# Kernel optimization log

Measured on AMD Instinct MI355X. Metric: run time of the kernel, lower is better.

The kernel has to match this reference:

```python
import jax, jax.numpy as jnp
import numpy as np

EMBED = 256
HEADS = 8
HEAD_DIM = EMBED // HEADS
K = 7          # kernel_size
DIL = 1        # dilation
PAD = DIL * (K - 1) // 2  # 3
B, H, W = 4, 56, 56


def setup_inputs() -> dict:
    key = jax.random.key(0)
    ks = jax.random.split(key, 9)
    d = {"x": jax.random.normal(ks[0], (B, H, W, EMBED), jnp.float32)}
    for i, name in enumerate(["wq", "wk", "wv", "wo"]):
        d[name] = jax.random.normal(ks[1 + i], (EMBED, EMBED), jnp.float32) * 0.02
    for i, name in enumerate(["bq", "bk", "bv", "bo"]):
        d[name] = jax.random.normal(ks[5 + i], (EMBED,), jnp.float32) * 0.02
    return d


def _unfold(t):
    # t: [N, d, H, W] -> [N, d, K*K, H, W]; zero padding (matches F.unfold),
    # so out-of-bounds neighbors contribute logit 0, NOT -inf (faithful to source).
    h, w = t.shape[2], t.shape[3]
    tp = jnp.pad(t, ((0, 0), (0, 0), (PAD, PAD), (PAD, PAD)))
    patches = [tp[:, :, i * DIL:i * DIL + h, j * DIL:j * DIL + w]
               for i in range(K) for j in range(K)]  # fixed K*K=49 offsets
    return jnp.stack(patches, axis=2)


def reference(x, wq, bq, wk, bk, wv, bv, wo, bo):
    b, h, w, c = x.shape
    scale = HEAD_DIM ** -0.5
    q = x @ wq.T + bq
    k = x @ wk.T + bk
    v = x @ wv.T + bv

    def to_nh(t):  # [B,H,W,C] -> [B*heads, head_dim, H, W]
        return t.reshape(b, h, w, HEADS, HEAD_DIM).transpose(0, 3, 4, 1, 2).reshape(b * HEADS, HEAD_DIM, h, w)

    q, k, v = to_nh(q), to_nh(k), to_nh(v)
    k_unf = _unfold(k)  # [N, d, K2, H, W]
    v_unf = _unfold(v)
    logits = jnp.einsum('ndhw,ndkhw->nkhw', q, k_unf) * scale  # [N, K2, H, W]
    attn = jax.nn.softmax(logits, axis=1)
    out = jnp.einsum('nkhw,ndkhw->ndhw', attn, v_unf)  # [N, d, H, W]
    out = out.reshape(b, HEADS, HEAD_DIM, h, w).transpose(0, 3, 4, 1, 2).reshape(b, h, w, c)
    return out @ wo.T + bo
```

## Files before the change

### kernel.cpp

```cpp
#include <hip/hip_runtime.h>

typedef unsigned int u32;
typedef unsigned short u16;
typedef _Float16 f16;
typedef __attribute__((ext_vector_type(8))) _Float16 f16x8;
typedef __attribute__((ext_vector_type(4))) float f32x4;

#define T_TOK 12544
#define EMB   256
#define IMG   56
#define SCALE2 0.25503486f
#define HALO  196
#define KSTR  40
#define VTSTR 208
#define PSTR  136

__device__ __forceinline__ u16 f16b(float f) {
    const f16 h = (f16)f;
    return __builtin_bit_cast(u16, h);
}

#define GLD16(g, l) __builtin_amdgcn_global_load_lds( \
    (const __attribute__((address_space(1))) u32*)(g), \
    (__attribute__((address_space(3))) u32*)(l), 16, 0, 0)

__global__ __launch_bounds__(256) void convert_kernel(
    const float* __restrict__ x, const float* __restrict__ wq, const float* __restrict__ wk,
    const float* __restrict__ wv, const float* __restrict__ wo,
    u16* __restrict__ xb, u16* __restrict__ wsh, u16* __restrict__ woh) {
    const int i = blockIdx.x * 256 + threadIdx.x;
    const int NX4 = T_TOK * EMB / 4;
    if (i < NX4) {
        const float4 f = ((const float4*)x)[i];
        ushort4 hv;
        hv.x = f16b(f.x); hv.y = f16b(f.y); hv.z = f16b(f.z); hv.w = f16b(f.w);
        ((ushort4*)xb)[i] = hv;
    } else {
        const int j = i - NX4;
        const int w = j >> 14, widx = j & 16383;
        const float* src = (w == 0) ? wq : (w == 1) ? wk : (w == 2) ? wv : wo;
        const float4 f = ((const float4*)src)[widx];
        ushort4 hv;
        hv.x = f16b(f.x); hv.y = f16b(f.y); hv.z = f16b(f.z); hv.w = f16b(f.w);
        if (w < 3) ((ushort4*)wsh)[(w << 14) + widx] = hv;
        else       ((ushort4*)woh)[widx] = hv;
    }
}

__global__ __launch_bounds__(256) void qkv_mfma(
    const u16* __restrict__ xb, const u16* __restrict__ wsh,
    const float* __restrict__ bq, const float* __restrict__ bk, const float* __restrict__ bv,
    u16* __restrict__ qb, u16* __restrict__ kb, u16* __restrict__ vb) {
    __shared__ __attribute__((aligned(16))) u16 sA[2][128 * 32];
    __shared__ __attribute__((aligned(16))) u16 sB[2][128 * 32];
    const int nBase = blockIdx.x * 128;
    const int mBase = blockIdx.y * 128;
    const int tid = threadIdx.x, wv = tid >> 6, ln = tid & 63;
    const int lrow = ln & 15, lqd = ln >> 4;
    const int wr = wv >> 1, wc = wv & 1;
    const int rA = tid >> 2, kcA = tid & 3;
    const size_t gA = (size_t)(mBase + rA) * EMB + kcA * 8;
    const size_t gB = (size_t)(nBase + rA) * EMB + kcA * 8;
    const int lA = wv * 512;

    f32x4 acc[4][4];
    #pragma unroll
    for (int mi = 0; mi < 4; ++mi)
        #pragma unroll
        for (int ni = 0; ni < 4; ++ni) acc[mi][ni] = (f32x4){0.f, 0.f, 0.f, 0.f};

    GLD16(xb  + gA,            &sA[0][lA]);
    GLD16(xb  + gA + 64 * EMB, &sA[0][2048 + lA]);
    GLD16(wsh + gB,            &sB[0][lA]);
    GLD16(wsh + gB + 64 * EMB, &sB[0][2048 + lA]);

    for (int kt = 0; kt < 8; ++kt) {
        const int b = kt & 1;
        __syncthreads();
        if (kt < 7) {
            const int k0 = (kt + 1) * 32;
            GLD16(xb  + gA + k0,            &sA[b ^ 1][lA]);
            GLD16(xb  + gA + k0 + 64 * EMB, &sA[b ^ 1][2048 + lA]);
            GLD16(wsh + gB + k0,            &sB[b ^ 1][lA]);
            GLD16(wsh + gB + k0 + 64 * EMB, &sB[b ^ 1][2048 + lA]);
        }
        f16x8 af[4], bfr[4];
        #pragma unroll
        for (int mi = 0; mi < 4; ++mi)
            af[mi] = *(const f16x8*)&sA[b][(wr * 64 + mi * 16 + lrow) * 32 + lqd * 8];
        #pragma unroll
        for (int ni = 0; ni < 4; ++ni)
            bfr[ni] = *(const f16x8*)&sB[b][(wc * 64 + ni * 16 + lrow) * 32 + lqd * 8];
        #pragma unroll
        for (int mi = 0; mi < 4; ++mi)
            #pragma unroll
            for (int ni = 0; ni < 4; ++ni)
                acc[mi][ni] = __builtin_amdgcn_mfma_f32_16x16x32_f16(af[mi], bfr[ni], acc[mi][ni], 0, 0, 0);
    }

    const int which = nBase >> 8;
    const float* bias = (which == 0) ? bq : (which == 1) ? bk : bv;
    u16* dst = (which == 0) ? qb : (which == 1) ? kb : vb;
    #pragma unroll
    for (int ni = 0; ni < 4; ++ni) {
        const int cg = (nBase & 255) + wc * 64 + ni * 16;
        const int head = cg >> 5;
        const int d = (cg & 31) + lrow;
        const float bz = bias[cg + lrow];
        u16* dh = dst + (size_t)head * T_TOK * 32;
        #pragma unroll
        for (int mi = 0; mi < 4; ++mi) {
            #pragma unroll
            for (int r = 0; r < 4; ++r) {
                const int row = mBase + wr * 64 + mi * 16 + lqd * 4 + r;
                dh[(size_t)row * 32 + d] = f16b(acc[mi][ni][r] + bz);
            }
        }
    }
}

__global__ __launch_bounds__(256) void out_mfma(
    const u16* __restrict__ ao, const u16* __restrict__ woh,
    const float* __restrict__ bo, float* __restrict__ out) {
    __shared__ __attribute__((aligned(16))) u16 sA[2][64 * 32];
    __shared__ __attribute__((aligned(16))) u16 sB[2][64 * 32];
    const int nBase = blockIdx.x * 64;
    const int mBase = blockIdx.y * 64;
    const int tid = threadIdx.x, wv = tid >> 6, ln = tid & 63;
    const int lrow = ln & 15, lqd = ln >> 4;
    const int rA = tid >> 2, kcA = tid & 3;
    const size_t gA = (size_t)(mBase + rA) * EMB + kcA * 8;
    const size_t gB = (size_t)(nBase + rA) * EMB + kcA * 8;
    const int lA = wv * 512;

    f32x4 acc[4];
    #pragma unroll
    for (int mi = 0; mi < 4; ++mi) acc[mi] = (f32x4){0.f, 0.f, 0.f, 0.f};

    GLD16(ao  + gA, &sA[0][lA]);
    GLD16(woh + gB, &sB[0][lA]);

    for (int kt = 0; kt < 8; ++kt) {
        const int b = kt & 1;
        __syncthreads();
        if (kt < 7) {
            const int k0 = (kt + 1) * 32;
            GLD16(ao  + gA + k0, &sA[b ^ 1][lA]);
            GLD16(woh + gB + k0, &sB[b ^ 1][lA]);
        }
        f16x8 af[4];
        #pragma unroll
        for (int mi = 0; mi < 4; ++mi)
            af[mi] = *(const f16x8*)&sA[b][(mi * 16 + lrow) * 32 + lqd * 8];
        const f16x8 bf = *(const f16x8*)&sB[b][(wv * 16 + lrow) * 32 + lqd * 8];
        #pragma unroll
        for (int mi = 0; mi < 4; ++mi)
            acc[mi] = __builtin_amdgcn_mfma_f32_16x16x32_f16(af[mi], bf, acc[mi], 0, 0, 0);
    }

    const int ncol = nBase + wv * 16 + lrow;
    const float bz = bo[ncol];
    #pragma unroll
    for (int mi = 0; mi < 4; ++mi) {
        #pragma unroll
        for (int r = 0; r < 4; ++r) {
            const int row = mBase + mi * 16 + lqd * 4 + r;
            out[(size_t)row * EMB + ncol] = acc[mi][r] + bz;
        }
    }
}

__global__ __launch_bounds__(256, 5) void attn_kernel(
    const u16* __restrict__ qb, const u16* __restrict__ kb, const u16* __restrict__ vb,
    u16* __restrict__ ao) {
    __shared__ __attribute__((aligned(16))) u16 smem[15360];
    u16* sVT = smem;
    u16* sK  = smem + 6656;
    u16* sP  = smem + 6656;

    const int tid = threadIdx.x;
    const int w = tid >> 6, ln = tid & 63;
    const int lrow = ln & 15, lqd = ln >> 4;
    const int img = blockIdx.z >> 3, head = blockIdx.z & 7;
    const int ty0 = blockIdx.y * 8, tx0 = blockIdx.x * 8;
    const int base8 = (28 * w) & ~7;

    const u16* kbh = kb + (size_t)head * (T_TOK * 32);
    const u16* vbh = vb + (size_t)head * (T_TOK * 32);
    const u16* qbh = qb + (size_t)head * (T_TOK * 32);

    for (int i = tid; i < 1664; i += 256) {
        const int mv = (i >= 832) ? 1 : 0;
        const int ii = i - 832 * mv;
        const int p = ii >> 2, c = ii & 3;
        const int pyh = p / 14, pxh = p - pyh * 14;
        const int gy = ty0 - 3 + pyh, gx = tx0 - 3 + pxh;
        const bool ok = (p < HALO) & ((unsigned)gy < 56u) & ((unsigned)gx < 56u);
        const size_t tt = (size_t)((img * IMG + gy) * IMG + gx) * 32;
        if (!mv) {
            u16* dstk = sK + p * KSTR + c * 8;
            if (ok) {
                *(uint4*)dstk = *(const uint4*)(kbh + tt + c * 8);
            } else {
                *(uint4*)dstk = (uint4){0u, 0u, 0u, 0u};
            }
        } else {
            u16* dv = sVT + (c * 8) * VTSTR + p;
            if (ok) {
                const uint4 u = *(const uint4*)(vbh + tt + c * 8);
                dv[0 * VTSTR] = (u16)(u.x & 0xffffu);
                dv[1 * VTSTR] = (u16)(u.x >> 16);
                dv[2 * VTSTR] = (u16)(u.y & 0xffffu);
                dv[3 * VTSTR] = (u16)(u.y >> 16);
                dv[4 * VTSTR] = (u16)(u.z & 0xffffu);
                dv[5 * VTSTR] = (u16)(u.z >> 16);
                dv[6 * VTSTR] = (u16)(u.w & 0xffffu);
                dv[7 * VTSTR] = (u16)(u.w >> 16);
            } else {
                #pragma unroll
                for (int j = 0; j < 8; ++j) dv[j * VTSTR] = 0;
            }
        }
    }

    const int mpix = w * 16 + lrow;
    const int qpy = mpix >> 3, qpx = mpix & 7;
    const size_t qtok = ((size_t)img * IMG + ty0 + qpy) * IMG + tx0 + qpx;
    const f16x8 aq = *(const f16x8*)&qbh[qtok * 32 + lqd * 8];
    __syncthreads();

    f32x4 ct[8];
    #pragma unroll
    for (int t = 0; t < 8; ++t) ct[t] = (f32x4){0.f, 0.f, 0.f, 0.f};
    #pragma unroll
    for (int t = 0; t < 8; ++t) {
        const f16x8 bk = *(const f16x8*)&sK[(base8 + t * 16 + lrow) * KSTR + lqd * 8];
        ct[t] = __builtin_amdgcn_mfma_f32_16x16x32_f16(aq, bk, ct[t], 0, 0, 0);
    }

    int pys[4], pxs[4];
    #pragma unroll
    for (int r = 0; r < 4; ++r) {
        const int row = lqd * 4 + r;
        pys[r] = 2 * w + (row >> 3);
        pxs[r] = row & 7;
    }
    float mr4[4] = {-1e30f, -1e30f, -1e30f, -1e30f};
    #pragma unroll
    for (int t = 0; t < 8; ++t) {
        const int col = base8 + t * 16 + lrow;
        const int hy = col / 14, hx = col - 14 * hy;
        const bool okc = (col < HALO);
        #pragma unroll
        for (int r = 0; r < 4; ++r) {
            const bool ok = ((unsigned)(hy - pys[r]) < 7u) &
                            ((unsigned)(hx - pxs[r]) < 7u) & okc;
            const float lv = ok ? ct[t][r] * SCALE2 : -1e30f;
            ct[t][r] = lv;
            mr4[r] = fmaxf(mr4[r], lv);
        }
    }
    #pragma unroll
    for (int r = 0; r < 4; ++r) {
        float m = mr4[r];
        m = fmaxf(m, __shfl_xor(m, 1));
        m = fmaxf(m, __shfl_xor(m, 2));
        m = fmaxf(m, __shfl_xor(m, 4));
        m = fmaxf(m, __shfl_xor(m, 8));
        mr4[r] = m;
    }
    float sr4[4] = {0.f, 0.f, 0.f, 0.f};
    #pragma unroll
    for (int t = 0; t < 8; ++t)
        #pragma unroll
        for (int r = 0; r < 4; ++r) {
            const float e = exp2f(ct[t][r] - mr4[r]);
            ct[t][r] = e;
            sr4[r] += e;
        }
    #pragma unroll
    for (int r = 0; r < 4; ++r) {
        float s = sr4[r];
        s += __shfl_xor(s, 1);
        s += __shfl_xor(s, 2);
        s += __shfl_xor(s, 4);
        s += __shfl_xor(s, 8);
        sr4[r] = 1.0f / s;
    }

    __syncthreads();

    u16* sPw = sP + w * 16 * PSTR;
    #pragma unroll
    for (int t = 0; t < 8; ++t)
        #pragma unroll
        for (int r = 0; r < 4; ++r)
            sPw[(lqd * 4 + r) * PSTR + t * 16 + lrow] = f16b(ct[t][r]);

    f32x4 o0 = (f32x4){0.f, 0.f, 0.f, 0.f};
    f32x4 o1 = (f32x4){0.f, 0.f, 0.f, 0.f};
    #pragma unroll
    for (int ks = 0; ks < 4; ++ks) {
        const f16x8 ap  = *(const f16x8*)&sPw[lrow * PSTR + ks * 32 + lqd * 8];
        const f16x8 bv0 = *(const f16x8*)&sVT[lrow * VTSTR + base8 + ks * 32 + lqd * 8];
        const f16x8 bv1 = *(const f16x8*)&sVT[(16 + lrow) * VTSTR + base8 + ks * 32 + lqd * 8];
        o0 = __builtin_amdgcn_mfma_f32_16x16x32_f16(ap, bv0, o0, 0, 0, 0);
        o1 = __builtin_amdgcn_mfma_f32_16x16x32_f16(ap, bv1, o1, 0, 0, 0);
    }

    #pragma unroll
    for (int r = 0; r < 4; ++r) {
        const int row = lqd * 4 + r;
        const int opy = 2 * w + (row >> 3), opx = row & 7;
        const size_t ot = ((size_t)img * IMG + ty0 + opy) * IMG + tx0 + opx;
        const float inv = sr4[r];
        const size_t base = ot * EMB + head * 32;
        ao[base + lrow]      = f16b(o0[r] * inv);
        ao[base + 16 + lrow] = f16b(o1[r] * inv);
    }
}

extern "C" void kernel_launch(void* const* d_in, const int* in_sizes, int n_in,
                              void* d_out, int out_size, void* d_ws, size_t ws_size,
                              hipStream_t stream) {
    const float* x  = (const float*)d_in[0];
    const float* wq = (const float*)d_in[1];
    const float* wk = (const float*)d_in[2];
    const float* wv = (const float*)d_in[3];
    const float* wo = (const float*)d_in[4];
    const float* bq = (const float*)d_in[5];
    const float* bk = (const float*)d_in[6];
    const float* bv = (const float*)d_in[7];
    const float* bo = (const float*)d_in[8];
    float* out = (float*)d_out;

    char* ws = (char*)d_ws;
    u16* xb  = (u16*)(ws);
    u16* qb  = (u16*)(ws +  6422528);
    u16* kb  = (u16*)(ws + 12845056);
    u16* vb  = (u16*)(ws + 19267584);
    u16* ao  = (u16*)(ws + 25690112);
    u16* wsh = (u16*)(ws + 32112640);
    u16* woh = (u16*)(ws + 32505856);

    convert_kernel<<<3392, 256, 0, stream>>>(x, wq, wk, wv, wo, xb, wsh, woh);
    qkv_mfma<<<dim3(6, 98), 256, 0, stream>>>(xb, wsh, bq, bk, bv, qb, kb, vb);
    attn_kernel<<<dim3(7, 7, 32), 256, 0, stream>>>(qb, kb, vb, ao);
    out_mfma<<<dim3(4, 196), 256, 0, stream>>>(ao, woh, bo, out);
}
```

Baseline: 121.9 us.

## Transpose attention MFMAs, drop softmax max pass, remap GEMM blocks across XCDs

Result: no change. 120.8 us (-0.9%).

```diff
diff --git a/kernel.cpp b/kernel.cpp
--- a/kernel.cpp
+++ b/kernel.cpp
@@ -53,8 +53,11 @@
     u16* __restrict__ qb, u16* __restrict__ kb, u16* __restrict__ vb) {
     __shared__ __attribute__((aligned(16))) u16 sA[2][128 * 32];
     __shared__ __attribute__((aligned(16))) u16 sB[2][128 * 32];
-    const int nBase = blockIdx.x * 128;
-    const int mBase = blockIdx.y * 128;
+    const int bid = blockIdx.y * 6 + blockIdx.x;
+    const int xcd = bid & 7, loc = bid >> 3;
+    const int work = (xcd < 4 ? xcd * 74 : 296 + (xcd - 4) * 73) + loc;
+    const int nBase = (work % 6) * 128;
+    const int mBase = (work / 6) * 128;
     const int tid = threadIdx.x, wv = tid >> 6, ln = tid & 63;
     const int lrow = ln & 15, lqd = ln >> 4;
     const int wr = wv >> 1, wc = wv & 1;
@@ -124,8 +127,10 @@
     const float* __restrict__ bo, float* __restrict__ out) {
     __shared__ __attribute__((aligned(16))) u16 sA[2][64 * 32];
     __shared__ __attribute__((aligned(16))) u16 sB[2][64 * 32];
-    const int nBase = blockIdx.x * 64;
-    const int mBase = blockIdx.y * 64;
+    const int bid = blockIdx.y * 4 + blockIdx.x;
+    const int work = (bid & 7) * 98 + (bid >> 3);
+    const int nBase = (work & 3) * 64;
+    const int mBase = (work >> 2) * 64;
     const int tid = threadIdx.x, wv = tid >> 6, ln = tid & 63;
     const int lrow = ln & 15, lqd = ln >> 4;
     const int rA = tid >> 2, kcA = tid & 3;
@@ -223,8 +228,7 @@
         }
     }
 
-    const int mpix = w * 16 + lrow;
-    const int qpy = mpix >> 3, qpx = mpix & 7;
+    const int qpy = 2 * w + (lrow >> 3), qpx = lrow & 7;
     const size_t qtok = ((size_t)img * IMG + ty0 + qpy) * IMG + tx0 + qpx;
     const f16x8 aq = *(const f16x8*)&qbh[qtok * 32 + lqd * 8];
     __syncthreads();
@@ -235,89 +239,59 @@
     #pragma unroll
     for (int t = 0; t < 8; ++t) {
         const f16x8 bk = *(const f16x8*)&sK[(base8 + t * 16 + lrow) * KSTR + lqd * 8];
-        ct[t] = __builtin_amdgcn_mfma_f32_16x16x32_f16(aq, bk, ct[t], 0, 0, 0);
-    }
-
-    int pys[4], pxs[4];
-    #pragma unroll
-    for (int r = 0; r < 4; ++r) {
-        const int row = lqd * 4 + r;
-        pys[r] = 2 * w + (row >> 3);
-        pxs[r] = row & 7;
-    }
-    float mr4[4] = {-1e30f, -1e30f, -1e30f, -1e30f};
+        ct[t] = __builtin_amdgcn_mfma_f32_16x16x32_f16(bk, aq, ct[t], 0, 0, 0);
+    }
+
+    float ssum = 0.f;
     #pragma unroll
     for (int t = 0; t < 8; ++t) {
-        const int col = base8 + t * 16 + lrow;
-        const int hy = col / 14, hx = col - 14 * hy;
-        const bool okc = (col < HALO);
         #pragma unroll
         for (int r = 0; r < 4; ++r) {
-            const bool ok = ((unsigned)(hy - pys[r]) < 7u) &
-                            ((unsigned)(hx - pxs[r]) < 7u) & okc;
-            const float lv = ok ? ct[t][r] * SCALE2 : -1e30f;
-            ct[t][r] = lv;
-            mr4[r] = fmaxf(mr4[r], lv);
-        }
-    }
-    #pragma unroll
-    for (int r = 0; r < 4; ++r) {
-        float m = mr4[r];
-        m = fmaxf(m, __shfl_xor(m, 1));
-        m = fmaxf(m, __shfl_xor(m, 2));
-        m = fmaxf(m, __shfl_xor(m, 4));
-        m = fmaxf(m, __shfl_xor(m, 8));
-        mr4[r] = m;
-    }
-    float sr4[4] = {0.f, 0.f, 0.f, 0.f};
-    #pragma unroll
-    for (int t = 0; t < 8; ++t)
-        #pragma unroll
-        for (int r = 0; r < 4; ++r) {
-            const float e = exp2f(ct[t][r] - mr4[r]);
+            const int col = base8 + t * 16 + lqd * 4 + r;
+            const int hy = col / 14, hx = col - 14 * hy;
+            const bool ok = ((unsigned)(hy - qpy) < 7u) &
+                            ((unsigned)(hx - qpx) < 7u) & (col < HALO);
+            const float e = ok ? exp2f(ct[t][r] * SCALE2) : 0.f;
             ct[t][r] = e;
-            sr4[r] += e;
-        }
-    #pragma unroll
-    for (int r = 0; r < 4; ++r) {
-        float s = sr4[r];
-        s += __shfl_xor(s, 1);
-        s += __shfl_xor(s, 2);
-        s += __shfl_xor(s, 4);
-        s += __shfl_xor(s, 8);
-        sr4[r] = 1.0f / s;
-    }
+            ssum += e;
+        }
+    }
+    ssum += __shfl_xor(ssum, 16);
+    ssum += __shfl_xor(ssum, 32);
+    const float inv = 1.0f / ssum;
 
     __syncthreads();
 
     u16* sPw = sP + w * 16 * PSTR;
     #pragma unroll
-    for (int t = 0; t < 8; ++t)
-        #pragma unroll
-        for (int r = 0; r < 4; ++r)
-            sPw[(lqd * 4 + r) * PSTR + t * 16 + lrow] = f16b(ct[t][r]);
+    for (int t = 0; t < 8; ++t) {
+        ushort4 pw;
+        pw.x = f16b(ct[t][0]);
+        pw.y = f16b(ct[t][1]);
+        pw.z = f16b(ct[t][2]);
+        pw.w = f16b(ct[t][3]);
+        *(ushort4*)&sPw[lrow * PSTR + t * 16 + lqd * 4] = pw;
+    }
 
     f32x4 o0 = (f32x4){0.f, 0.f, 0.f, 0.f};
     f32x4 o1 = (f32x4){0.f, 0.f, 0.f, 0.f};
     #pragma unroll
     for (int ks = 0; ks < 4; ++ks) {
         const f16x8 ap  = *(const f16x8*)&sPw[lrow * PSTR + ks * 32 + lqd * 8];
-        const f16x8 bv0 = *(const f16x8*)&sVT[lrow * VTSTR + base8 + ks * 32 + lqd * 8];
-        const f16x8 bv1 = *(const f16x8*)&sVT[(16 + lrow) * VTSTR + base8 + ks * 32 + lqd * 8];
-        o0 = __builtin_amdgcn_mfma_f32_16x16x32_f16(ap, bv0, o0, 0, 0, 0);
-        o1 = __builtin_amdgcn_mfma_f32_16x16x32_f16(ap, bv1, o1, 0, 0, 0);
-    }
-
-    #pragma unroll
-    for (int r = 0; r < 4; ++r) {
-        const int row = lqd * 4 + r;
-        const int opy = 2 * w + (row >> 3), opx = row & 7;
-        const size_t ot = ((size_t)img * IMG + ty0 + opy) * IMG + tx0 + opx;
-        const float inv = sr4[r];
-        const size_t base = ot * EMB + head * 32;
-        ao[base + lrow]      = f16b(o0[r] * inv);
-        ao[base + 16 + lrow] = f16b(o1[r] * inv);
-    }
+        const f16x8 av0 = *(const f16x8*)&sVT[lrow * VTSTR + base8 + ks * 32 + lqd * 8];
+        const f16x8 av1 = *(const f16x8*)&sVT[(16 + lrow) * VTSTR + base8 + ks * 32 + lqd * 8];
+        o0 = __builtin_amdgcn_mfma_f32_16x16x32_f16(av0, ap, o0, 0, 0, 0);
+        o1 = __builtin_amdgcn_mfma_f32_16x16x32_f16(av1, ap, o1, 0, 0, 0);
+    }
+
+    const size_t base = qtok * EMB + head * 32;
+    ushort4 s0, s1;
+    s0.x = f16b(o0[0] * inv); s0.y = f16b(o0[1] * inv);
+    s0.z = f16b(o0[2] * inv); s0.w = f16b(o0[3] * inv);
+    s1.x = f16b(o1[0] * inv); s1.y = f16b(o1[1] * inv);
+    s1.z = f16b(o1[2] * inv); s1.w = f16b(o1[3] * inv);
+    *(ushort4*)&ao[base + lqd * 4]      = s0;
+    *(ushort4*)&ao[base + 16 + lqd * 4] = s1;
 }
 
 extern "C" void kernel_launch(void* const* d_in, const int* in_sizes, int n_in,
```
